# Performance work log

Hardware: AMD Instinct MI355X
Metric: run time of the kernel (lower is better)

Reference implementation:

```python
import jax, jax.numpy as jnp
import numpy as np

K = 2  # num_experts_used (top-k)


def setup_inputs() -> dict:
    key = jax.random.key(0)
    ks = jax.random.split(key, 6)
    B, S, D, U, E = 2, 2048, 1024, 4096, 8
    return {
        "x": jax.random.normal(ks[0], (B, S, D), dtype=jnp.float32),
        "w_router": jax.random.normal(ks[1], (E, D), dtype=jnp.float32),
        "w_up": jax.random.normal(ks[2], (E, U, D), dtype=jnp.float32),
        "b_up": jax.random.normal(ks[3], (E, U), dtype=jnp.float32),
        "w_down": jax.random.normal(ks[4], (E, D, U), dtype=jnp.float32),
        "b_down": jax.random.normal(ks[5], (E, D), dtype=jnp.float32),
    }


def reference(x, w_router, w_up, b_up, w_down, b_down):
    # Router: Linear(embed_dim -> num_experts), no bias
    logits = jnp.einsum('bsd,ed->bse', x, w_router)
    top_logits, idx = jax.lax.top_k(logits, K)          # [b,s,k]
    router_weights = jax.nn.softmax(top_logits, axis=-1)  # softmax over top-k logits

    # Compute all-expert FFN outputs (same math as per-token gathered weights,
    # without materializing the (b,s,k,u,d) weight copies of the original).
    h = jnp.einsum('eud,bsd->bseu', w_up, x) + b_up[None, None]   # [b,s,E,u]
    h = jax.nn.gelu(h, approximate=False)
    y = jnp.einsum('edu,bseu->bsed', w_down, h) + b_down[None, None]  # [b,s,E,d]

    # Gather outputs of the top-k experts per token
    y_k = jnp.take_along_axis(y, idx[..., None], axis=2)  # [b,s,k,d]
    out = jnp.einsum('bskd,bsk->bsd', y_k, router_weights)
    return out
```

## Files before the change

kernel.cpp:

```cpp
#include <hip/hip_runtime.h>
#include <hip/hip_bf16.h>
#include <stdint.h>
#include <math.h>

#define TTOK 4096
#define DDIM 1024
#define UDIM 4096
#define NEXP 8
#define KSPLIT 2
#define KCH   (UDIM / KSPLIT)
#define NPAIR (TTOK * 2)
#define EPAD 72

using float4v = __attribute__((ext_vector_type(4))) float;
using short8  = __attribute__((ext_vector_type(8))) short;
using ushort8 = __attribute__((ext_vector_type(8))) unsigned short;

__device__ __forceinline__ unsigned short f2bf(float f) {
  union { float f; unsigned u; } v; v.f = f;
  unsigned r = v.u + 0x7FFFu + ((v.u >> 16) & 1u);
  return (unsigned short)(r >> 16);
}
__device__ __forceinline__ float bf2f(unsigned short u) {
  union { unsigned u; float f; } v; v.u = ((unsigned)u) << 16;
  return v.f;
}
__device__ __forceinline__ void load_lds16(const void* g, void* l) {
  __builtin_amdgcn_global_load_lds(
      (const __attribute__((address_space(1))) unsigned int*)g,
      (__attribute__((address_space(3))) unsigned int*)l, 16, 0, 0);
}
__device__ __forceinline__ short8 cvt8(const float4v a, const float4v b) {
  union { __hip_bfloat162 h[4]; short8 s; } u;
  u.h[0] = __float22bfloat162_rn(make_float2(a[0], a[1]));
  u.h[1] = __float22bfloat162_rn(make_float2(a[2], a[3]));
  u.h[2] = __float22bfloat162_rn(make_float2(b[0], b[1]));
  u.h[3] = __float22bfloat162_rn(make_float2(b[2], b[3]));
  return u.s;
}
__device__ __forceinline__ float gelu_f(float v) {
  float u = v * (0.7978845608f + 0.0356774081f * v * v);
  float ex = __expf(2.0f * u);
  return v * (1.0f - 1.0f / (1.0f + ex));
}

__global__ void router_kernel(const float* __restrict__ x,
                              const float* __restrict__ wr,
                              int* __restrict__ counts, int* __restrict__ list,
                              float* __restrict__ wpair, int* __restrict__ epair,
                              unsigned short* __restrict__ xb) {
  const int t = blockIdx.x * 4 + (threadIdx.x >> 6);
  const int lane = threadIdx.x & 63;
  float acc[NEXP];
#pragma unroll
  for (int e = 0; e < NEXP; e++) acc[e] = 0.0f;
  const float* xr = x + (size_t)t * DDIM;
  unsigned short* xbr = xb + (size_t)t * DDIM;
  for (int d = lane; d < DDIM; d += 64) {
    float xv = xr[d];
    xbr[d] = f2bf(xv);
#pragma unroll
    for (int e = 0; e < NEXP; e++) acc[e] += xv * wr[e * DDIM + d];
  }
#pragma unroll
  for (int e = 0; e < NEXP; e++) {
#pragma unroll
    for (int off = 32; off > 0; off >>= 1) acc[e] += __shfl_xor(acc[e], off, 64);
  }
  if (lane == 0) {
    int e0 = 0; float l0 = acc[0];
    for (int e = 1; e < NEXP; e++) if (acc[e] > l0) { l0 = acc[e]; e0 = e; }
    int e1 = -1; float l1 = -3.4e38f;
    for (int e = 0; e < NEXP; e++) if (e != e0 && acc[e] > l1) { l1 = acc[e]; e1 = e; }
    float s1 = expf(l1 - l0);
    float inv = 1.0f / (1.0f + s1);
    int p0 = atomicAdd(&counts[e0], 1);
    list[e0 * TTOK + p0] = 2 * t;
    wpair[2 * t] = inv;  epair[2 * t] = e0;
    int p1 = atomicAdd(&counts[e1], 1);
    list[e1 * TTOK + p1] = 2 * t + 1;
    wpair[2 * t + 1] = s1 * inv;  epair[2 * t + 1] = e1;
  }
}

__global__ __launch_bounds__(256, 3) void stage_up_k(
    const unsigned short* __restrict__ xb, const float* __restrict__ wu,
    const float* __restrict__ bup, const int* __restrict__ counts,
    const int* __restrict__ list, unsigned short* __restrict__ h) {
  const int e = blockIdx.z, mt = blockIdx.y, nt = blockIdx.x;
  const int cnt = counts[e];
  if (mt * 128 >= cnt) return;
  const int rem = min(128, cnt - mt * 128);
  const int* lst = list + e * TTOK + mt * 128;

  __shared__ __align__(16) char SM[24576];
  unsigned short* Sb = (unsigned short*)SM;

  const int tid = threadIdx.x;
  const int wave = tid >> 6, lane = tid & 63;
  const int srow = tid >> 2, cell = tid & 3;
  const int brow = tid >> 3;
  const int bswz = (tid & 7) ^ (brow & 7);

  const int tok0 = lst[min(srow, rem - 1)] >> 1;
  const int tok1 = lst[min(srow + 64, rem - 1)] >> 1;
  const unsigned short* a0 = xb + (size_t)tok0 * DDIM + cell * 8;
  const unsigned short* a1 = xb + (size_t)tok1 * DDIM + cell * 8;
  const float* bbase = wu + ((size_t)e * UDIM + nt * 128) * DDIM;
  const float* bsrc[4];
#pragma unroll
  for (int k = 0; k < 4; k++) bsrc[k] = bbase + (size_t)(brow + k * 32) * DDIM + bswz * 4;

  const int wm = wave >> 1, wn = wave & 1;
  const int lane15 = lane & 15, quad = lane >> 4;
  const int abyte = (wm * 64 + lane15) * 64 + quad * 16;
  const int p0 = (2 * quad) ^ (lane & 7);
  const int bbyte = 8192 + (wn * 64 + lane15) * 128;

  float4v acc[4][4];
#pragma unroll
  for (int i = 0; i < 4; i++)
#pragma unroll
    for (int j = 0; j < 4; j++) acc[i][j] = (float4v){0.f, 0.f, 0.f, 0.f};

  for (int k0 = 0; k0 < DDIM; k0 += 32) {
    load_lds16(a0 + k0, SM + tid * 16);
    load_lds16(a1 + k0, SM + 4096 + tid * 16);
#pragma unroll
    for (int k = 0; k < 4; k++) load_lds16(bsrc[k] + k0, SM + 8192 + k * 4096 + tid * 16);
    __syncthreads();
    short8 af[4], bfr[4];
#pragma unroll
    for (int mi = 0; mi < 4; mi++) af[mi] = *(const short8*)(SM + abyte + mi * 1024);
#pragma unroll
    for (int ni = 0; ni < 4; ni++) {
      const char* rb = SM + bbyte + ni * 2048;
      float4v f0 = *(const float4v*)(rb + p0 * 16);
      float4v f1 = *(const float4v*)(rb + (p0 ^ 1) * 16);
      bfr[ni] = cvt8(f0, f1);
    }
#pragma unroll
    for (int mi = 0; mi < 4; mi++)
#pragma unroll
      for (int ni = 0; ni < 4; ni++)
        acc[mi][ni] = __builtin_amdgcn_mfma_f32_16x16x32_bf16(af[mi], bfr[ni], acc[mi][ni], 0, 0, 0);
    __syncthreads();
  }

  const int ucol0 = nt * 128 + wn * 64;
  float bias[4];
#pragma unroll
  for (int ni = 0; ni < 4; ni++) bias[ni] = bup[e * UDIM + ucol0 + ni * 16 + lane15];
  const int row = tid >> 1, seg = tid & 1;
  const int opair = (row < rem) ? lst[row] : -1;
#pragma unroll
  for (int hh = 0; hh < 2; hh++) {
    if (wn == hh) {
#pragma unroll
      for (int mi = 0; mi < 4; mi++)
#pragma unroll
        for (int r = 0; r < 4; r++) {
          const int rl = wm * 64 + mi * 16 + quad * 4 + r;
#pragma unroll
          for (int ni = 0; ni < 4; ni++)
            Sb[rl * EPAD + ni * 16 + lane15] = f2bf(gelu_f(acc[mi][ni][r] + bias[ni]));
        }
    }
    __syncthreads();
    if (opair >= 0) {
      unsigned short* dst = h + (size_t)opair * UDIM + nt * 128 + hh * 64 + seg * 32;
      const unsigned short* src = Sb + row * EPAD + seg * 32;
#pragma unroll
      for (int c = 0; c < 4; c++) *(ushort8*)(dst + c * 8) = *(const ushort8*)(src + c * 8);
    }
    __syncthreads();
  }
}

template <bool PARTM>
__global__ __launch_bounds__(256, 3) void stage_down_k(
    const unsigned short* __restrict__ h, const float* __restrict__ wd,
    const float* __restrict__ bdn, const float* __restrict__ wpair,
    const int* __restrict__ counts, const int* __restrict__ list,
    unsigned short* __restrict__ part, float* __restrict__ out) {
  const int e = blockIdx.z, mt = blockIdx.y >> 1, kc = blockIdx.y & 1, nt = blockIdx.x;
  const int cnt = counts[e];
  if (mt * 128 >= cnt) return;
  const int rem = min(128, cnt - mt * 128);
  const int* lst = list + e * TTOK + mt * 128;

  __shared__ __align__(16) char SM[24576];
  unsigned short* Sb = (unsigned short*)SM;

  const int tid = threadIdx.x;
  const int wave = tid >> 6, lane = tid & 63;
  const int srow = tid >> 2, cell = tid & 3;
  const int brow = tid >> 3;
  const int bswz = (tid & 7) ^ (brow & 7);

  const int pr0 = lst[min(srow, rem - 1)];
  const int pr1 = lst[min(srow + 64, rem - 1)];
  const unsigned short* a0 = h + (size_t)pr0 * UDIM + kc * KCH + cell * 8;
  const unsigned short* a1 = h + (size_t)pr1 * UDIM + kc * KCH + cell * 8;
  const float* bbase = wd + ((size_t)e * DDIM + nt * 128) * UDIM + kc * KCH;
  const float* bsrc[4];
#pragma unroll
  for (int k = 0; k < 4; k++) bsrc[k] = bbase + (size_t)(brow + k * 32) * UDIM + bswz * 4;

  const int wm = wave >> 1, wn = wave & 1;
  const int lane15 = lane & 15, quad = lane >> 4;
  const int abyte = (wm * 64 + lane15) * 64 + quad * 16;
  const int p0 = (2 * quad) ^ (lane & 7);
  const int bbyte = 8192 + (wn * 64 + lane15) * 128;

  float4v acc[4][4];
#pragma unroll
  for (int i = 0; i < 4; i++)
#pragma unroll
    for (int j = 0; j < 4; j++) acc[i][j] = (float4v){0.f, 0.f, 0.f, 0.f};

  for (int k0 = 0; k0 < KCH; k0 += 32) {
    load_lds16(a0 + k0, SM + tid * 16);
    load_lds16(a1 + k0, SM + 4096 + tid * 16);
#pragma unroll
    for (int k = 0; k < 4; k++) load_lds16(bsrc[k] + k0, SM + 8192 + k * 4096 + tid * 16);
    __syncthreads();
    short8 af[4], bfr[4];
#pragma unroll
    for (int mi = 0; mi < 4; mi++) af[mi] = *(const short8*)(SM + abyte + mi * 1024);
#pragma unroll
    for (int ni = 0; ni < 4; ni++) {
      const char* rb = SM + bbyte + ni * 2048;
      float4v f0 = *(const float4v*)(rb + p0 * 16);
      float4v f1 = *(const float4v*)(rb + (p0 ^ 1) * 16);
      bfr[ni] = cvt8(f0, f1);
    }
#pragma unroll
    for (int mi = 0; mi < 4; mi++)
#pragma unroll
      for (int ni = 0; ni < 4; ni++)
        acc[mi][ni] = __builtin_amdgcn_mfma_f32_16x16x32_bf16(af[mi], bfr[ni], acc[mi][ni], 0, 0, 0);
    __syncthreads();
  }

  const int dcol0 = nt * 128 + wn * 64;
  if constexpr (PARTM) {
    const int row = tid >> 1, seg = tid & 1;
    const int opair = (row < rem) ? lst[row] : -1;
#pragma unroll
    for (int hh = 0; hh < 2; hh++) {
      if (wn == hh) {
#pragma unroll
        for (int mi = 0; mi < 4; mi++)
#pragma unroll
          for (int r = 0; r < 4; r++) {
            const int rl = wm * 64 + mi * 16 + quad * 4 + r;
#pragma unroll
            for (int ni = 0; ni < 4; ni++)
              Sb[rl * EPAD + ni * 16 + lane15] = f2bf(acc[mi][ni][r]);
          }
      }
      __syncthreads();
      if (opair >= 0) {
        unsigned short* dst = part + ((size_t)kc * NPAIR + opair) * DDIM + nt * 128 + hh * 64 + seg * 32;
        const unsigned short* src = Sb + row * EPAD + seg * 32;
#pragma unroll
        for (int c = 0; c < 4; c++) *(ushort8*)(dst + c * 8) = *(const ushort8*)(src + c * 8);
      }
      __syncthreads();
    }
  } else {
    float bias[4];
#pragma unroll
    for (int ni = 0; ni < 4; ni++)
      bias[ni] = (kc == 0) ? bdn[e * DDIM + dcol0 + ni * 16 + lane15] : 0.0f;
#pragma unroll
    for (int mi = 0; mi < 4; mi++)
#pragma unroll
      for (int r = 0; r < 4; r++) {
        const int mrow = wm * 64 + mi * 16 + quad * 4 + r;
        if (mrow < rem) {
          const int pair = lst[mrow];
          const float w = wpair[pair];
          float* orow = out + (size_t)(pair >> 1) * DDIM;
#pragma unroll
          for (int ni = 0; ni < 4; ni++)
            atomicAdd(&orow[dcol0 + ni * 16 + lane15], w * (acc[mi][ni][r] + bias[ni]));
        }
      }
  }
}

__global__ void combine_kernel(const unsigned short* __restrict__ part,
                               const float* __restrict__ bdn,
                               const float* __restrict__ wpair,
                               const int* __restrict__ epair,
                               float* __restrict__ out) {
  const int idx = blockIdx.x * 256 + threadIdx.x;
  const int t = idx >> 7, c8 = (idx & 127) * 8;
  const size_t kstride = (size_t)NPAIR * DDIM;
  const unsigned short* pa = part + (size_t)(2 * t) * DDIM + c8;
  float s0[8], s1[8];
#pragma unroll
  for (int j = 0; j < 8; j++) { s0[j] = 0.f; s1[j] = 0.f; }
#pragma unroll
  for (int kc = 0; kc < KSPLIT; kc++) {
    ushort8 a = *(const ushort8*)(pa + kc * kstride);
    ushort8 b = *(const ushort8*)(pa + kc * kstride + DDIM);
#pragma unroll
    for (int j = 0; j < 8; j++) { s0[j] += bf2f(a[j]); s1[j] += bf2f(b[j]); }
  }
  const float w0 = wpair[2 * t], w1 = wpair[2 * t + 1];
  const int e0 = epair[2 * t], e1 = epair[2 * t + 1];
  const float* b0 = bdn + e0 * DDIM + c8;
  const float* b1 = bdn + e1 * DDIM + c8;
  float4v o[2];
#pragma unroll
  for (int half = 0; half < 2; half++)
#pragma unroll
    for (int j = 0; j < 4; j++) {
      const int jj = half * 4 + j;
      o[half][j] = w0 * (s0[jj] + b0[jj]) + w1 * (s1[jj] + b1[jj]);
    }
  float4v* dst = (float4v*)(out + (size_t)t * DDIM + c8);
  dst[0] = o[0]; dst[1] = o[1];
}

__global__ void zero_out_k(float4v* __restrict__ out) {
  const int tid = blockIdx.x * blockDim.x + threadIdx.x;
  const int O4 = TTOK * DDIM / 4;
  const int stride = gridDim.x * blockDim.x;
  for (int i = tid; i < O4; i += stride) out[i] = (float4v){0.f, 0.f, 0.f, 0.f};
}

extern "C" void kernel_launch(void* const* d_in, const int* in_sizes, int n_in,
                              void* d_out, int out_size, void* d_ws, size_t ws_size,
                              hipStream_t stream) {
  (void)in_sizes; (void)n_in; (void)out_size;
  const float* x        = (const float*)d_in[0];
  const float* w_router = (const float*)d_in[1];
  const float* w_up     = (const float*)d_in[2];
  const float* b_up     = (const float*)d_in[3];
  const float* w_down   = (const float*)d_in[4];
  const float* b_down   = (const float*)d_in[5];
  float* out = (float*)d_out;

  char* ws = (char*)d_ws;
  size_t off = 0;
  auto take = [&](size_t b) { size_t o = off; off = (off + b + 255) & ~(size_t)255; return o; };
  unsigned short* h  = (unsigned short*)(ws + take((size_t)NPAIR * UDIM * 2));
  unsigned short* xb = (unsigned short*)(ws + take((size_t)TTOK * DDIM * 2));
  int* counts        = (int*)(ws + take(NEXP * 4));
  int* list          = (int*)(ws + take((size_t)NEXP * TTOK * 4));
  float* wpair       = (float*)(ws + take((size_t)NPAIR * 4));
  int* epair         = (int*)(ws + take((size_t)NPAIR * 4));
  size_t part_off    = take((size_t)KSPLIT * NPAIR * DDIM * 2);
  const bool partmode = ws_size >= off;

  hipMemsetAsync(counts, 0, NEXP * 4, stream);
  router_kernel<<<TTOK / 4, 256, 0, stream>>>(x, w_router, counts, list, wpair, epair, xb);
  stage_up_k<<<dim3(UDIM / 128, 32, NEXP), 256, 0, stream>>>(xb, w_up, b_up, counts, list, h);

  if (partmode) {
    unsigned short* part = (unsigned short*)(ws + part_off);
    stage_down_k<true><<<dim3(DDIM / 128, 32 * KSPLIT, NEXP), 256, 0, stream>>>(
        h, w_down, b_down, wpair, counts, list, part, out);
    combine_kernel<<<TTOK * DDIM / 8 / 256, 256, 0, stream>>>(part, b_down, wpair, epair, out);
  } else {
    zero_out_k<<<1024, 256, 0, stream>>>((float4v*)out);
    stage_down_k<false><<<dim3(DDIM / 128, 32 * KSPLIT, NEXP), 256, 0, stream>>>(
        h, w_down, b_down, wpair, counts, list, (unsigned short*)nullptr, out);
  }
}
```

Before: 667.9 us.

## Pre-convert expert weights to bf16 in a fused prep kernel before GEMMs

Adds a prep kernel that runs the router and, in spare blocks, converts all up and down expert weights from fp32 to bf16 in workspace. New up/down GEMM kernels then load bf16 weights directly into LDS with async global_load_lds instead of converting fp32 weights inside the GEMM loop. This halves GEMM weight traffic and removes the in-loop conversion, but it adds a full conversion pass over 256MB of fp32 weights every call and needs 128MB of extra workspace. The new path is only taken when the workspace is large enough.

```diff
diff --git a/kernel.cpp b/kernel.cpp
--- a/kernel.cpp
+++ b/kernel.cpp
@@ -44,13 +44,11 @@
   return v * (1.0f - 1.0f / (1.0f + ex));
 }
 
-__global__ void router_kernel(const float* __restrict__ x,
-                              const float* __restrict__ wr,
-                              int* __restrict__ counts, int* __restrict__ list,
-                              float* __restrict__ wpair, int* __restrict__ epair,
-                              unsigned short* __restrict__ xb) {
-  const int t = blockIdx.x * 4 + (threadIdx.x >> 6);
-  const int lane = threadIdx.x & 63;
+__device__ __forceinline__ void router_body(
+    int t, int lane, const float* __restrict__ x, const float* __restrict__ wr,
+    int* __restrict__ counts, int* __restrict__ list,
+    float* __restrict__ wpair, int* __restrict__ epair,
+    unsigned short* __restrict__ xb) {
   float acc[NEXP];
 #pragma unroll
   for (int e = 0; e < NEXP; e++) acc[e] = 0.0f;
@@ -83,6 +81,205 @@
   }
 }
 
+__global__ void router_kernel(const float* __restrict__ x,
+                              const float* __restrict__ wr,
+                              int* __restrict__ counts, int* __restrict__ list,
+                              float* __restrict__ wpair, int* __restrict__ epair,
+                              unsigned short* __restrict__ xb) {
+  const int t = blockIdx.x * 4 + (threadIdx.x >> 6);
+  router_body(t, threadIdx.x & 63, x, wr, counts, list, wpair, epair, xb);
+}
+
+__global__ void prep_kernel(const float* __restrict__ x, const float* __restrict__ wr,
+                            int* __restrict__ counts, int* __restrict__ list,
+                            float* __restrict__ wpair, int* __restrict__ epair,
+                            unsigned short* __restrict__ xb,
+                            const float* __restrict__ wu, const float* __restrict__ wd,
+                            unsigned short* __restrict__ wub, unsigned short* __restrict__ wdb) {
+  const int bid = blockIdx.x;
+  if (bid < TTOK / 4) {
+    const int t = bid * 4 + (threadIdx.x >> 6);
+    router_body(t, threadIdx.x & 63, x, wr, counts, list, wpair, epair, xb);
+    return;
+  }
+  const size_t n8 = (size_t)NEXP * UDIM * DDIM / 8;
+  const size_t cb = (size_t)(bid - TTOK / 4);
+  const size_t stride = (size_t)(gridDim.x - TTOK / 4) * 256;
+  for (size_t i = cb * 256 + threadIdx.x; i < 2 * n8; i += stride) {
+    const float* s; unsigned short* d;
+    if (i < n8) { s = wu + i * 8; d = wub + i * 8; }
+    else        { s = wd + (i - n8) * 8; d = wdb + (i - n8) * 8; }
+    float4v lo = *(const float4v*)s;
+    float4v hi = *(const float4v*)(s + 4);
+    short8 v = cvt8(lo, hi);
+    *(short8*)d = v;
+  }
+}
+
+__global__ __launch_bounds__(256, 4) void stage_up_b16(
+    const unsigned short* __restrict__ xb, const unsigned short* __restrict__ wub,
+    const float* __restrict__ bup, const int* __restrict__ counts,
+    const int* __restrict__ list, unsigned short* __restrict__ h) {
+  const int e = blockIdx.z, mt = blockIdx.y, nt = blockIdx.x;
+  const int cnt = counts[e];
+  if (mt * 128 >= cnt) return;
+  const int rem = min(128, cnt - mt * 128);
+  const int* lst = list + e * TTOK + mt * 128;
+
+  __shared__ __align__(16) char SM[18432];
+  unsigned short* Sb = (unsigned short*)SM;
+
+  const int tid = threadIdx.x;
+  const int wave = tid >> 6, lane = tid & 63;
+  const int srow = tid >> 2, cell = tid & 3;
+
+  const int tok0 = lst[min(srow, rem - 1)] >> 1;
+  const int tok1 = lst[min(srow + 64, rem - 1)] >> 1;
+  const unsigned short* a0 = xb + (size_t)tok0 * DDIM + cell * 8;
+  const unsigned short* a1 = xb + (size_t)tok1 * DDIM + cell * 8;
+  const unsigned short* b0 = wub + ((size_t)e * UDIM + nt * 128 + srow) * DDIM + cell * 8;
+  const unsigned short* b1 = b0 + (size_t)64 * DDIM;
+
+  const int wm = wave >> 1, wn = wave & 1;
+  const int lane15 = lane & 15, quad = lane >> 4;
+  const int abyte = (wm * 64 + lane15) * 64 + quad * 16;
+  const int bbyte = 8192 + (wn * 64 + lane15) * 64 + quad * 16;
+
+  float4v acc[4][4];
+#pragma unroll
+  for (int i = 0; i < 4; i++)
+#pragma unroll
+    for (int j = 0; j < 4; j++) acc[i][j] = (float4v){0.f, 0.f, 0.f, 0.f};
+
+  for (int k0 = 0; k0 < DDIM; k0 += 32) {
+    load_lds16(a0 + k0, SM + tid * 16);
+    load_lds16(a1 + k0, SM + 4096 + tid * 16);
+    load_lds16(b0 + k0, SM + 8192 + tid * 16);
+    load_lds16(b1 + k0, SM + 12288 + tid * 16);
+    __syncthreads();
+    short8 af[4], bfr[4];
+#pragma unroll
+    for (int mi = 0; mi < 4; mi++) af[mi] = *(const short8*)(SM + abyte + mi * 1024);
+#pragma unroll
+    for (int ni = 0; ni < 4; ni++) bfr[ni] = *(const short8*)(SM + bbyte + ni * 1024);
+#pragma unroll
+    for (int mi = 0; mi < 4; mi++)
+#pragma unroll
+      for (int ni = 0; ni < 4; ni++)
+        acc[mi][ni] = __builtin_amdgcn_mfma_f32_16x16x32_bf16(af[mi], bfr[ni], acc[mi][ni], 0, 0, 0);
+    __syncthreads();
+  }
+
+  const int ucol0 = nt * 128 + wn * 64;
+  float bias[4];
+#pragma unroll
+  for (int ni = 0; ni < 4; ni++) bias[ni] = bup[e * UDIM + ucol0 + ni * 16 + lane15];
+  const int row = tid >> 1, seg = tid & 1;
+  const int opair = (row < rem) ? lst[row] : -1;
+#pragma unroll
+  for (int hh = 0; hh < 2; hh++) {
+    if (wn == hh) {
+#pragma unroll
+      for (int mi = 0; mi < 4; mi++)
+#pragma unroll
+        for (int r = 0; r < 4; r++) {
+          const int rl = wm * 64 + mi * 16 + quad * 4 + r;
+#pragma unroll
+          for (int ni = 0; ni < 4; ni++)
+            Sb[rl * EPAD + ni * 16 + lane15] = f2bf(gelu_f(acc[mi][ni][r] + bias[ni]));
+        }
+    }
+    __syncthreads();
+    if (opair >= 0) {
+      unsigned short* dst = h + (size_t)opair * UDIM + nt * 128 + hh * 64 + seg * 32;
+      const unsigned short* src = Sb + row * EPAD + seg * 32;
+#pragma unroll
+      for (int c = 0; c < 4; c++) *(ushort8*)(dst + c * 8) = *(const ushort8*)(src + c * 8);
+    }
+    __syncthreads();
+  }
+}
+
+__global__ __launch_bounds__(256, 4) void stage_down_b16(
+    const unsigned short* __restrict__ h, const unsigned short* __restrict__ wdb,
+    const int* __restrict__ counts, const int* __restrict__ list,
+    unsigned short* __restrict__ part) {
+  const int e = blockIdx.z, mt = blockIdx.y >> 1, kc = blockIdx.y & 1, nt = blockIdx.x;
+  const int cnt = counts[e];
+  if (mt * 128 >= cnt) return;
+  const int rem = min(128, cnt - mt * 128);
+  const int* lst = list + e * TTOK + mt * 128;
+
+  __shared__ __align__(16) char SM[18432];
+  unsigned short* Sb = (unsigned short*)SM;
+
+  const int tid = threadIdx.x;
+  const int wave = tid >> 6, lane = tid & 63;
+  const int srow = tid >> 2, cell = tid & 3;
+
+  const int pr0 = lst[min(srow, rem - 1)];
+  const int pr1 = lst[min(srow + 64, rem - 1)];
+  const unsigned short* a0 = h + (size_t)pr0 * UDIM + kc * KCH + cell * 8;
+  const unsigned short* a1 = h + (size_t)pr1 * UDIM + kc * KCH + cell * 8;
+  const unsigned short* b0 = wdb + ((size_t)e * DDIM + nt * 128 + srow) * UDIM + kc * KCH + cell * 8;
+  const unsigned short* b1 = b0 + (size_t)64 * UDIM;
+
+  const int wm = wave >> 1, wn = wave & 1;
+  const int lane15 = lane & 15, quad = lane >> 4;
+  const int abyte = (wm * 64 + lane15) * 64 + quad * 16;
+  const int bbyte = 8192 + (wn * 64 + lane15) * 64 + quad * 16;
+
+  float4v acc[4][4];
+#pragma unroll
+  for (int i = 0; i < 4; i++)
+#pragma unroll
+    for (int j = 0; j < 4; j++) acc[i][j] = (float4v){0.f, 0.f, 0.f, 0.f};
+
+  for (int k0 = 0; k0 < KCH; k0 += 32) {
+    load_lds16(a0 + k0, SM + tid * 16);
+    load_lds16(a1 + k0, SM + 4096 + tid * 16);
+    load_lds16(b0 + k0, SM + 8192 + tid * 16);
+    load_lds16(b1 + k0, SM + 12288 + tid * 16);
+    __syncthreads();
+    short8 af[4], bfr[4];
+#pragma unroll
+    for (int mi = 0; mi < 4; mi++) af[mi] = *(const short8*)(SM + abyte + mi * 1024);
+#pragma unroll
+    for (int ni = 0; ni < 4; ni++) bfr[ni] = *(const short8*)(SM + bbyte + ni * 1024);
+#pragma unroll
+    for (int mi = 0; mi < 4; mi++)
+#pragma unroll
+      for (int ni = 0; ni < 4; ni++)
+        acc[mi][ni] = __builtin_amdgcn_mfma_f32_16x16x32_bf16(af[mi], bfr[ni], acc[mi][ni], 0, 0, 0);
+    __syncthreads();
+  }
+
+  const int row = tid >> 1, seg = tid & 1;
+  const int opair = (row < rem) ? lst[row] : -1;
+#pragma unroll
+  for (int hh = 0; hh < 2; hh++) {
+    if (wn == hh) {
+#pragma unroll
+      for (int mi = 0; mi < 4; mi++)
+#pragma unroll
+        for (int r = 0; r < 4; r++) {
+          const int rl = wm * 64 + mi * 16 + quad * 4 + r;
+#pragma unroll
+          for (int ni = 0; ni < 4; ni++)
+            Sb[rl * EPAD + ni * 16 + lane15] = f2bf(acc[mi][ni][r]);
+        }
+    }
+    __syncthreads();
+    if (opair >= 0) {
+      unsigned short* dst = part + ((size_t)kc * NPAIR + opair) * DDIM + nt * 128 + hh * 64 + seg * 32;
+      const unsigned short* src = Sb + row * EPAD + seg * 32;
+#pragma unroll
+      for (int c = 0; c < 4; c++) *(ushort8*)(dst + c * 8) = *(const ushort8*)(src + c * 8);
+    }
+    __syncthreads();
+  }
+}
+
 __global__ __launch_bounds__(256, 3) void stage_up_k(
     const unsigned short* __restrict__ xb, const float* __restrict__ wu,
     const float* __restrict__ bup, const int* __restrict__ counts,
@@ -356,19 +553,35 @@
   int* epair         = (int*)(ws + take((size_t)NPAIR * 4));
   size_t part_off    = take((size_t)KSPLIT * NPAIR * DDIM * 2);
   const bool partmode = ws_size >= off;
+  size_t wub_off     = take((size_t)NEXP * UDIM * DDIM * 2);
+  size_t wdb_off     = take((size_t)NEXP * DDIM * UDIM * 2);
+  const bool bf16mode = ws_size >= off;
 
   hipMemsetAsync(counts, 0, NEXP * 4, stream);
-  router_kernel<<<TTOK / 4, 256, 0, stream>>>(x, w_router, counts, list, wpair, epair, xb);
-  stage_up_k<<<dim3(UDIM / 128, 32, NEXP), 256, 0, stream>>>(xb, w_up, b_up, counts, list, h);
-
-  if (partmode) {
+
+  if (bf16mode) {
     unsigned short* part = (unsigned short*)(ws + part_off);
-    stage_down_k<true><<<dim3(DDIM / 128, 32 * KSPLIT, NEXP), 256, 0, stream>>>(
-        h, w_down, b_down, wpair, counts, list, part, out);
+    unsigned short* wub  = (unsigned short*)(ws + wub_off);
+    unsigned short* wdb  = (unsigned short*)(ws + wdb_off);
+    prep_kernel<<<TTOK / 4 + 2048, 256, 0, stream>>>(
+        x, w_router, counts, list, wpair, epair, xb, w_up, w_down, wub, wdb);
+    stage_up_b16<<<dim3(UDIM / 128, 32, NEXP), 256, 0, stream>>>(
+        xb, wub, b_up, counts, list, h);
+    stage_down_b16<<<dim3(DDIM / 128, 32 * KSPLIT, NEXP), 256, 0, stream>>>(
+        h, wdb, counts, list, part);
     combine_kernel<<<TTOK * DDIM / 8 / 256, 256, 0, stream>>>(part, b_down, wpair, epair, out);
   } else {
-    zero_out_k<<<1024, 256, 0, stream>>>((float4v*)out);
-    stage_down_k<false><<<dim3(DDIM / 128, 32 * KSPLIT, NEXP), 256, 0, stream>>>(
-        h, w_down, b_down, wpair, counts, list, (unsigned short*)nullptr, out);
-  }
-}
+    router_kernel<<<TTOK / 4, 256, 0, stream>>>(x, w_router, counts, list, wpair, epair, xb);
+    stage_up_k<<<dim3(UDIM / 128, 32, NEXP), 256, 0, stream>>>(xb, w_up, b_up, counts, list, h);
+    if (partmode) {
+      unsigned short* part = (unsigned short*)(ws + part_off);
+      stage_down_k<true><<<dim3(DDIM / 128, 32 * KSPLIT, NEXP), 256, 0, stream>>>(
+          h, w_down, b_down, wpair, counts, list, part, out);
+      combine_kernel<<<TTOK * DDIM / 8 / 256, 256, 0, stream>>>(part, b_down, wpair, epair, out);
+    } else {
+      zero_out_k<<<1024, 256, 0, stream>>>((float4v*)out);
+      stage_down_k<false><<<dim3(DDIM / 128, 32 * KSPLIT, NEXP), 256, 0, stream>>>(
+          h, w_down, b_down, wpair, counts, list, (unsigned short*)nullptr, out);
+    }
+  }
+}
```

New measurement: 651.9 us. 2.4% less time.

## Convert fp32 weights to bf16 in registers before LDS, batch router atomics

Applied to the files above, without the earlier changes.

The up and down GEMMs now load fp32 weight tiles into registers with a one-step register prefetch, convert them to bf16, and store bf16 into LDS. This halves LDS footprint and removes the per-wave fp32 LDS reads and repeated conversions. The router handles 16 tokens per block with vectorized loads and aggregates per-expert counts in shared memory, so it issues one atomic per expert with counters padded apart. The down-stage grid is reordered so that M tiles vary fastest, and occupancy hints are raised to 4 blocks. The trade-off is that weight loads no longer use the async global-to-LDS path, so latency hiding depends on the register prefetch.

```diff
diff --git a/kernel.cpp b/kernel.cpp
--- a/kernel.cpp
+++ b/kernel.cpp
@@ -11,10 +11,13 @@
 #define KCH   (UDIM / KSPLIT)
 #define NPAIR (TTOK * 2)
 #define EPAD 72
+#define CPAD 32
+#define RTOK 16
 
 using float4v = __attribute__((ext_vector_type(4))) float;
 using short8  = __attribute__((ext_vector_type(8))) short;
 using ushort8 = __attribute__((ext_vector_type(8))) unsigned short;
+using ushort4v = __attribute__((ext_vector_type(4))) unsigned short;
 
 __device__ __forceinline__ unsigned short f2bf(float f) {
   union { float f; unsigned u; } v; v.f = f;
@@ -49,73 +52,100 @@
                               int* __restrict__ counts, int* __restrict__ list,
                               float* __restrict__ wpair, int* __restrict__ epair,
                               unsigned short* __restrict__ xb) {
-  const int t = blockIdx.x * 4 + (threadIdx.x >> 6);
-  const int lane = threadIdx.x & 63;
-  float acc[NEXP];
-#pragma unroll
-  for (int e = 0; e < NEXP; e++) acc[e] = 0.0f;
-  const float* xr = x + (size_t)t * DDIM;
-  unsigned short* xbr = xb + (size_t)t * DDIM;
-  for (int d = lane; d < DDIM; d += 64) {
-    float xv = xr[d];
-    xbr[d] = f2bf(xv);
-#pragma unroll
-    for (int e = 0; e < NEXP; e++) acc[e] += xv * wr[e * DDIM + d];
-  }
-#pragma unroll
-  for (int e = 0; e < NEXP; e++) {
-#pragma unroll
-    for (int off = 32; off > 0; off >>= 1) acc[e] += __shfl_xor(acc[e], off, 64);
-  }
-  if (lane == 0) {
-    int e0 = 0; float l0 = acc[0];
-    for (int e = 1; e < NEXP; e++) if (acc[e] > l0) { l0 = acc[e]; e0 = e; }
-    int e1 = -1; float l1 = -3.4e38f;
-    for (int e = 0; e < NEXP; e++) if (e != e0 && acc[e] > l1) { l1 = acc[e]; e1 = e; }
-    float s1 = expf(l1 - l0);
-    float inv = 1.0f / (1.0f + s1);
-    int p0 = atomicAdd(&counts[e0], 1);
-    list[e0 * TTOK + p0] = 2 * t;
-    wpair[2 * t] = inv;  epair[2 * t] = e0;
-    int p1 = atomicAdd(&counts[e1], 1);
-    list[e1 * TTOK + p1] = 2 * t + 1;
-    wpair[2 * t + 1] = s1 * inv;  epair[2 * t + 1] = e1;
-  }
-}
-
-__global__ __launch_bounds__(256, 3) void stage_up_k(
+  __shared__ int sE0[RTOK], sE1[RTOK];
+  const int bid = blockIdx.x;
+  const int tid = threadIdx.x;
+  const int wave = tid >> 6, lane = tid & 63;
+#pragma unroll 1
+  for (int j = 0; j < RTOK / 4; j++) {
+    const int slot = wave * (RTOK / 4) + j;
+    const int t = bid * RTOK + slot;
+    float acc[NEXP];
+#pragma unroll
+    for (int e = 0; e < NEXP; e++) acc[e] = 0.0f;
+    const float* xr = x + (size_t)t * DDIM;
+    unsigned short* xbr = xb + (size_t)t * DDIM;
+#pragma unroll
+    for (int it = 0; it < 4; it++) {
+      const int d = it * 256 + lane * 4;
+      float4v xv = *(const float4v*)(xr + d);
+      ushort4v xo;
+#pragma unroll
+      for (int c = 0; c < 4; c++) xo[c] = f2bf(xv[c]);
+      *(ushort4v*)(xbr + d) = xo;
+#pragma unroll
+      for (int e = 0; e < NEXP; e++) {
+        float4v wv = *(const float4v*)(wr + e * DDIM + d);
+        acc[e] += xv[0] * wv[0] + xv[1] * wv[1] + xv[2] * wv[2] + xv[3] * wv[3];
+      }
+    }
+#pragma unroll
+    for (int e = 0; e < NEXP; e++) {
+#pragma unroll
+      for (int off = 32; off > 0; off >>= 1) acc[e] += __shfl_xor(acc[e], off, 64);
+    }
+    if (lane == 0) {
+      int e0 = 0; float l0 = acc[0];
+      for (int e = 1; e < NEXP; e++) if (acc[e] > l0) { l0 = acc[e]; e0 = e; }
+      int e1 = -1; float l1 = -3.4e38f;
+      for (int e = 0; e < NEXP; e++) if (e != e0 && acc[e] > l1) { l1 = acc[e]; e1 = e; }
+      float s1 = expf(l1 - l0);
+      float inv = 1.0f / (1.0f + s1);
+      wpair[2 * t] = inv;          epair[2 * t] = e0;
+      wpair[2 * t + 1] = s1 * inv; epair[2 * t + 1] = e1;
+      sE0[slot] = e0;  sE1[slot] = e1;
+    }
+  }
+  __syncthreads();
+  if (tid < NEXP) {
+    const int e = tid;
+    int cnt = 0;
+#pragma unroll
+    for (int s = 0; s < RTOK; s++) cnt += (sE0[s] == e) + (sE1[s] == e);
+    int r = atomicAdd(&counts[e * CPAD], cnt);
+    int* le = list + e * TTOK;
+#pragma unroll 1
+    for (int s = 0; s < RTOK; s++) {
+      const int p = 2 * (bid * RTOK + s);
+      if (sE0[s] == e) le[r++] = p;
+      if (sE1[s] == e) le[r++] = p + 1;
+    }
+  }
+}
+
+__global__ __launch_bounds__(256, 4) void stage_up_rs(
     const unsigned short* __restrict__ xb, const float* __restrict__ wu,
     const float* __restrict__ bup, const int* __restrict__ counts,
     const int* __restrict__ list, unsigned short* __restrict__ h) {
   const int e = blockIdx.z, mt = blockIdx.y, nt = blockIdx.x;
-  const int cnt = counts[e];
+  const int cnt = counts[e * CPAD];
   if (mt * 128 >= cnt) return;
   const int rem = min(128, cnt - mt * 128);
   const int* lst = list + e * TTOK + mt * 128;
 
-  __shared__ __align__(16) char SM[24576];
+  __shared__ __align__(16) char SM[18432];
   unsigned short* Sb = (unsigned short*)SM;
 
   const int tid = threadIdx.x;
   const int wave = tid >> 6, lane = tid & 63;
   const int srow = tid >> 2, cell = tid & 3;
-  const int brow = tid >> 3;
-  const int bswz = (tid & 7) ^ (brow & 7);
 
   const int tok0 = lst[min(srow, rem - 1)] >> 1;
   const int tok1 = lst[min(srow + 64, rem - 1)] >> 1;
   const unsigned short* a0 = xb + (size_t)tok0 * DDIM + cell * 8;
   const unsigned short* a1 = xb + (size_t)tok1 * DDIM + cell * 8;
-  const float* bbase = wu + ((size_t)e * UDIM + nt * 128) * DDIM;
-  const float* bsrc[4];
-#pragma unroll
-  for (int k = 0; k < 4; k++) bsrc[k] = bbase + (size_t)(brow + k * 32) * DDIM + bswz * 4;
+  const float* bw0 = wu + ((size_t)e * UDIM + nt * 128 + srow) * DDIM + cell * 8;
+  const float* bw1 = bw0 + (size_t)64 * DDIM;
 
   const int wm = wave >> 1, wn = wave & 1;
   const int lane15 = lane & 15, quad = lane >> 4;
   const int abyte = (wm * 64 + lane15) * 64 + quad * 16;
-  const int p0 = (2 * quad) ^ (lane & 7);
-  const int bbyte = 8192 + (wn * 64 + lane15) * 128;
+  const int bbyte = 8192 + (wn * 64 + lane15) * 64 + quad * 16;
+
+  float4v p00 = *(const float4v*)(bw0);
+  float4v p01 = *(const float4v*)(bw0 + 4);
+  float4v p10 = *(const float4v*)(bw1);
+  float4v p11 = *(const float4v*)(bw1 + 4);
 
   float4v acc[4][4];
 #pragma unroll
@@ -126,19 +156,22 @@
   for (int k0 = 0; k0 < DDIM; k0 += 32) {
     load_lds16(a0 + k0, SM + tid * 16);
     load_lds16(a1 + k0, SM + 4096 + tid * 16);
-#pragma unroll
-    for (int k = 0; k < 4; k++) load_lds16(bsrc[k] + k0, SM + 8192 + k * 4096 + tid * 16);
+    short8 bv0 = cvt8(p00, p01);
+    short8 bv1 = cvt8(p10, p11);
+    if (k0 + 32 < DDIM) {
+      p00 = *(const float4v*)(bw0 + k0 + 32);
+      p01 = *(const float4v*)(bw0 + k0 + 36);
+      p10 = *(const float4v*)(bw1 + k0 + 32);
+      p11 = *(const float4v*)(bw1 + k0 + 36);
+    }
+    *(short8*)(SM + 8192 + tid * 16) = bv0;
+    *(short8*)(SM + 12288 + tid * 16) = bv1;
     __syncthreads();
     short8 af[4], bfr[4];
 #pragma unroll
     for (int mi = 0; mi < 4; mi++) af[mi] = *(const short8*)(SM + abyte + mi * 1024);
 #pragma unroll
-    for (int ni = 0; ni < 4; ni++) {
-      const char* rb = SM + bbyte + ni * 2048;
-      float4v f0 = *(const float4v*)(rb + p0 * 16);
-      float4v f1 = *(const float4v*)(rb + (p0 ^ 1) * 16);
-      bfr[ni] = cvt8(f0, f1);
-    }
+    for (int ni = 0; ni < 4; ni++) bfr[ni] = *(const short8*)(SM + bbyte + ni * 1024);
 #pragma unroll
     for (int mi = 0; mi < 4; mi++)
 #pragma unroll
@@ -177,41 +210,132 @@
   }
 }
 
-template <bool PARTM>
+__global__ __launch_bounds__(256, 4) void stage_down_rs(
+    const unsigned short* __restrict__ h, const float* __restrict__ wd,
+    const int* __restrict__ counts, const int* __restrict__ list,
+    unsigned short* __restrict__ part) {
+  const int e = blockIdx.z, mt = blockIdx.x >> 1, kc = blockIdx.x & 1, nt = blockIdx.y;
+  const int cnt = counts[e * CPAD];
+  if (mt * 128 >= cnt) return;
+  const int rem = min(128, cnt - mt * 128);
+  const int* lst = list + e * TTOK + mt * 128;
+
+  __shared__ __align__(16) char SM[18432];
+  unsigned short* Sb = (unsigned short*)SM;
+
+  const int tid = threadIdx.x;
+  const int wave = tid >> 6, lane = tid & 63;
+  const int srow = tid >> 2, cell = tid & 3;
+
+  const int pr0 = lst[min(srow, rem - 1)];
+  const int pr1 = lst[min(srow + 64, rem - 1)];
+  const unsigned short* a0 = h + (size_t)pr0 * UDIM + kc * KCH + cell * 8;
+  const unsigned short* a1 = h + (size_t)pr1 * UDIM + kc * KCH + cell * 8;
+  const float* bw0 = wd + ((size_t)e * DDIM + nt * 128 + srow) * UDIM + kc * KCH + cell * 8;
+  const float* bw1 = bw0 + (size_t)64 * UDIM;
+
+  const int wm = wave >> 1, wn = wave & 1;
+  const int lane15 = lane & 15, quad = lane >> 4;
+  const int abyte = (wm * 64 + lane15) * 64 + quad * 16;
+  const int bbyte = 8192 + (wn * 64 + lane15) * 64 + quad * 16;
+
+  float4v p00 = *(const float4v*)(bw0);
+  float4v p01 = *(const float4v*)(bw0 + 4);
+  float4v p10 = *(const float4v*)(bw1);
+  float4v p11 = *(const float4v*)(bw1 + 4);
+
+  float4v acc[4][4];
+#pragma unroll
+  for (int i = 0; i < 4; i++)
+#pragma unroll
+    for (int j = 0; j < 4; j++) acc[i][j] = (float4v){0.f, 0.f, 0.f, 0.f};
+
+  for (int k0 = 0; k0 < KCH; k0 += 32) {
+    load_lds16(a0 + k0, SM + tid * 16);
+    load_lds16(a1 + k0, SM + 4096 + tid * 16);
+    short8 bv0 = cvt8(p00, p01);
+    short8 bv1 = cvt8(p10, p11);
+    if (k0 + 32 < KCH) {
+      p00 = *(const float4v*)(bw0 + k0 + 32);
+      p01 = *(const float4v*)(bw0 + k0 + 36);
+      p10 = *(const float4v*)(bw1 + k0 + 32);
+      p11 = *(const float4v*)(bw1 + k0 + 36);
+    }
+    *(short8*)(SM + 8192 + tid * 16) = bv0;
+    *(short8*)(SM + 12288 + tid * 16) = bv1;
+    __syncthreads();
+    short8 af[4], bfr[4];
+#pragma unroll
+    for (int mi = 0; mi < 4; mi++) af[mi] = *(const short8*)(SM + abyte + mi * 1024);
+#pragma unroll
+    for (int ni = 0; ni < 4; ni++) bfr[ni] = *(const short8*)(SM + bbyte + ni * 1024);
+#pragma unroll
+    for (int mi = 0; mi < 4; mi++)
+#pragma unroll
+      for (int ni = 0; ni < 4; ni++)
+        acc[mi][ni] = __builtin_amdgcn_mfma_f32_16x16x32_bf16(af[mi], bfr[ni], acc[mi][ni], 0, 0, 0);
+    __syncthreads();
+  }
+
+  const int row = tid >> 1, seg = tid & 1;
+  const int opair = (row < rem) ? lst[row] : -1;
+#pragma unroll
+  for (int hh = 0; hh < 2; hh++) {
+    if (wn == hh) {
+#pragma unroll
+      for (int mi = 0; mi < 4; mi++)
+#pragma unroll
+        for (int r = 0; r < 4; r++) {
+          const int rl = wm * 64 + mi * 16 + quad * 4 + r;
+#pragma unroll
+          for (int ni = 0; ni < 4; ni++)
+            Sb[rl * EPAD + ni * 16 + lane15] = f2bf(acc[mi][ni][r]);
+        }
+    }
+    __syncthreads();
+    if (opair >= 0) {
+      unsigned short* dst = part + ((size_t)kc * NPAIR + opair) * DDIM + nt * 128 + hh * 64 + seg * 32;
+      const unsigned short* src = Sb + row * EPAD + seg * 32;
+#pragma unroll
+      for (int c = 0; c < 4; c++) *(ushort8*)(dst + c * 8) = *(const ushort8*)(src + c * 8);
+    }
+    __syncthreads();
+  }
+}
+
 __global__ __launch_bounds__(256, 3) void stage_down_k(
     const unsigned short* __restrict__ h, const float* __restrict__ wd,
     const float* __restrict__ bdn, const float* __restrict__ wpair,
     const int* __restrict__ counts, const int* __restrict__ list,
-    unsigned short* __restrict__ part, float* __restrict__ out) {
+    float* __restrict__ out) {
   const int e = blockIdx.z, mt = blockIdx.y >> 1, kc = blockIdx.y & 1, nt = blockIdx.x;
-  const int cnt = counts[e];
+  const int cnt = counts[e * CPAD];
   if (mt * 128 >= cnt) return;
   const int rem = min(128, cnt - mt * 128);
   const int* lst = list + e * TTOK + mt * 128;
 
-  __shared__ __align__(16) char SM[24576];
-  unsigned short* Sb = (unsigned short*)SM;
+  __shared__ __align__(16) char SM[18432];
 
   const int tid = threadIdx.x;
   const int wave = tid >> 6, lane = tid & 63;
   const int srow = tid >> 2, cell = tid & 3;
-  const int brow = tid >> 3;
-  const int bswz = (tid & 7) ^ (brow & 7);
 
   const int pr0 = lst[min(srow, rem - 1)];
   const int pr1 = lst[min(srow + 64, rem - 1)];
   const unsigned short* a0 = h + (size_t)pr0 * UDIM + kc * KCH + cell * 8;
   const unsigned short* a1 = h + (size_t)pr1 * UDIM + kc * KCH + cell * 8;
-  const float* bbase = wd + ((size_t)e * DDIM + nt * 128) * UDIM + kc * KCH;
-  const float* bsrc[4];
-#pragma unroll
-  for (int k = 0; k < 4; k++) bsrc[k] = bbase + (size_t)(brow + k * 32) * UDIM + bswz * 4;
+  const float* bw0 = wd + ((size_t)e * DDIM + nt * 128 + srow) * UDIM + kc * KCH + cell * 8;
+  const float* bw1 = bw0 + (size_t)64 * UDIM;
 
   const int wm = wave >> 1, wn = wave & 1;
   const int lane15 = lane & 15, quad = lane >> 4;
   const int abyte = (wm * 64 + lane15) * 64 + quad * 16;
-  const int p0 = (2 * quad) ^ (lane & 7);
-  const int bbyte = 8192 + (wn * 64 + lane15) * 128;
+  const int bbyte = 8192 + (wn * 64 + lane15) * 64 + quad * 16;
+
+  float4v p00 = *(const float4v*)(bw0);
+  float4v p01 = *(const float4v*)(bw0 + 4);
+  float4v p10 = *(const float4v*)(bw1);
+  float4v p11 = *(const float4v*)(bw1 + 4);
 
   float4v acc[4][4];
 #pragma unroll
@@ -222,19 +346,22 @@
   for (int k0 = 0; k0 < KCH; k0 += 32) {
     load_lds16(a0 + k0, SM + tid * 16);
     load_lds16(a1 + k0, SM + 4096 + tid * 16);
-#pragma unroll
-    for (int k = 0; k < 4; k++) load_lds16(bsrc[k] + k0, SM + 8192 + k * 4096 + tid * 16);
+    short8 bv0 = cvt8(p00, p01);
+    short8 bv1 = cvt8(p10, p11);
+    if (k0 + 32 < KCH) {
+      p00 = *(const float4v*)(bw0 + k0 + 32);
+      p01 = *(const float4v*)(bw0 + k0 + 36);
+      p10 = *(const float4v*)(bw1 + k0 + 32);
+      p11 = *(const float4v*)(bw1 + k0 + 36);
+    }
+    *(short8*)(SM + 8192 + tid * 16) = bv0;
+    *(short8*)(SM + 12288 + tid * 16) = bv1;
     __syncthreads();
     short8 af[4], bfr[4];
 #pragma unroll
     for (int mi = 0; mi < 4; mi++) af[mi] = *(const short8*)(SM + abyte + mi * 1024);
 #pragma unroll
-    for (int ni = 0; ni < 4; ni++) {
-      const char* rb = SM + bbyte + ni * 2048;
-      float4v f0 = *(const float4v*)(rb + p0 * 16);
-      float4v f1 = *(const float4v*)(rb + (p0 ^ 1) * 16);
-      bfr[ni] = cvt8(f0, f1);
-    }
+    for (int ni = 0; ni < 4; ni++) bfr[ni] = *(const short8*)(SM + bbyte + ni * 1024);
 #pragma unroll
     for (int mi = 0; mi < 4; mi++)
 #pragma unroll
@@ -244,51 +371,24 @@
   }
 
   const int dcol0 = nt * 128 + wn * 64;
-  if constexpr (PARTM) {
-    const int row = tid >> 1, seg = tid & 1;
-    const int opair = (row < rem) ? lst[row] : -1;
-#pragma unroll
-    for (int hh = 0; hh < 2; hh++) {
-      if (wn == hh) {
-#pragma unroll
-        for (int mi = 0; mi < 4; mi++)
-#pragma unroll
-          for (int r = 0; r < 4; r++) {
-            const int rl = wm * 64 + mi * 16 + quad * 4 + r;
-#pragma unroll
-            for (int ni = 0; ni < 4; ni++)
-              Sb[rl * EPAD + ni * 16 + lane15] = f2bf(acc[mi][ni][r]);
-          }
+  float bias[4];
+#pragma unroll
+  for (int ni = 0; ni < 4; ni++)
+    bias[ni] = (kc == 0) ? bdn[e * DDIM + dcol0 + ni * 16 + lane15] : 0.0f;
+#pragma unroll
+  for (int mi = 0; mi < 4; mi++)
+#pragma unroll
+    for (int r = 0; r < 4; r++) {
+      const int mrow = wm * 64 + mi * 16 + quad * 4 + r;
+      if (mrow < rem) {
+        const int pair = lst[mrow];
+        const float w = wpair[pair];
+        float* orow = out + (size_t)(pair >> 1) * DDIM;
+#pragma unroll
+        for (int ni = 0; ni < 4; ni++)
+          atomicAdd(&orow[dcol0 + ni * 16 + lane15], w * (acc[mi][ni][r] + bias[ni]));
       }
-      __syncthreads();
-      if (opair >= 0) {
-        unsigned short* dst = part + ((size_t)kc * NPAIR + opair) * DDIM + nt * 128 + hh * 64 + seg * 32;
-        const unsigned short* src = Sb + row * EPAD + seg * 32;
-#pragma unroll
-        for (int c = 0; c < 4; c++) *(ushort8*)(dst + c * 8) = *(const ushort8*)(src + c * 8);
-      }
-      __syncthreads();
-    }
-  } else {
-    float bias[4];
-#pragma unroll
-    for (int ni = 0; ni < 4; ni++)
-      bias[ni] = (kc == 0) ? bdn[e * DDIM + dcol0 + ni * 16 + lane15] : 0.0f;
-#pragma unroll
-    for (int mi = 0; mi < 4; mi++)
-#pragma unroll
-      for (int r = 0; r < 4; r++) {
-        const int mrow = wm * 64 + mi * 16 + quad * 4 + r;
-        if (mrow < rem) {
-          const int pair = lst[mrow];
-          const float w = wpair[pair];
-          float* orow = out + (size_t)(pair >> 1) * DDIM;
-#pragma unroll
-          for (int ni = 0; ni < 4; ni++)
-            atomicAdd(&orow[dcol0 + ni * 16 + lane15], w * (acc[mi][ni][r] + bias[ni]));
-        }
-      }
-  }
+    }
 }
 
 __global__ void combine_kernel(const unsigned short* __restrict__ part,
@@ -350,25 +450,26 @@
   auto take = [&](size_t b) { size_t o = off; off = (off + b + 255) & ~(size_t)255; return o; };
   unsigned short* h  = (unsigned short*)(ws + take((size_t)NPAIR * UDIM * 2));
   unsigned short* xb = (unsigned short*)(ws + take((size_t)TTOK * DDIM * 2));
-  int* counts        = (int*)(ws + take(NEXP * 4));
+  int* counts        = (int*)(ws + take(NEXP * CPAD * 4));
   int* list          = (int*)(ws + take((size_t)NEXP * TTOK * 4));
   float* wpair       = (float*)(ws + take((size_t)NPAIR * 4));
   int* epair         = (int*)(ws + take((size_t)NPAIR * 4));
   size_t part_off    = take((size_t)KSPLIT * NPAIR * DDIM * 2);
   const bool partmode = ws_size >= off;
 
-  hipMemsetAsync(counts, 0, NEXP * 4, stream);
-  router_kernel<<<TTOK / 4, 256, 0, stream>>>(x, w_router, counts, list, wpair, epair, xb);
-  stage_up_k<<<dim3(UDIM / 128, 32, NEXP), 256, 0, stream>>>(xb, w_up, b_up, counts, list, h);
+  hipMemsetAsync(counts, 0, NEXP * CPAD * 4, stream);
+
+  router_kernel<<<TTOK / RTOK, 256, 0, stream>>>(x, w_router, counts, list, wpair, epair, xb);
+  stage_up_rs<<<dim3(UDIM / 128, 32, NEXP), 256, 0, stream>>>(xb, w_up, b_up, counts, list, h);
 
   if (partmode) {
     unsigned short* part = (unsigned short*)(ws + part_off);
-    stage_down_k<true><<<dim3(DDIM / 128, 32 * KSPLIT, NEXP), 256, 0, stream>>>(
-        h, w_down, b_down, wpair, counts, list, part, out);
+    stage_down_rs<<<dim3(32 * KSPLIT, DDIM / 128, NEXP), 256, 0, stream>>>(
+        h, w_down, counts, list, part);
     combine_kernel<<<TTOK * DDIM / 8 / 256, 256, 0, stream>>>(part, b_down, wpair, epair, out);
   } else {
     zero_out_k<<<1024, 256, 0, stream>>>((float4v*)out);
-    stage_down_k<false><<<dim3(DDIM / 128, 32 * KSPLIT, NEXP), 256, 0, stream>>>(
-        h, w_down, b_down, wpair, counts, list, (unsigned short*)nullptr, out);
-  }
-}
+    stage_down_k<<<dim3(DDIM / 128, 32 * KSPLIT, NEXP), 256, 0, stream>>>(
+        h, w_down, b_down, wpair, counts, list, out);
+  }
+}
```

After: 633.2 us. -5.2%, faster.
